# Kernel tuning notes

Measured on AMD Instinct MI355X. Metric: run time of the kernel, lower is better.

## Reference

```python
import jax, jax.numpy as jnp
import numpy as np

B, C, H, W = 4, 256, 64, 64
CH = C // 2  # inner channels


def setup_inputs() -> dict:
    key = jax.random.key(0)
    ks = jax.random.split(key, 9)
    s_in = 1.0 / np.sqrt(C)
    s_w = 1.0 / np.sqrt(CH)
    return {
        "x": jax.random.normal(ks[0], (B, C, H, W), dtype=jnp.float32),
        "theta_w": jax.random.normal(ks[1], (CH, C), dtype=jnp.float32) * s_in,
        "theta_b": jax.random.normal(ks[2], (CH,), dtype=jnp.float32) * s_in,
        "phi_w": jax.random.normal(ks[3], (CH, C), dtype=jnp.float32) * s_in,
        "phi_b": jax.random.normal(ks[4], (CH,), dtype=jnp.float32) * s_in,
        "g_w": jax.random.normal(ks[5], (CH, C), dtype=jnp.float32) * s_in,
        "g_b": jax.random.normal(ks[6], (CH,), dtype=jnp.float32) * s_in,
        "W_w": jax.random.normal(ks[7], (C, CH), dtype=jnp.float32) * s_w,
        "W_b": jax.random.normal(ks[8], (C,), dtype=jnp.float32) * s_w,
    }


def _proj(x_flat, w, b):
    # 1x1 conv == channel matmul; x_flat: [B, C, N] -> [B, O, N]
    return jnp.einsum("oc,bcn->bon", w, x_flat) + b[None, :, None]


def reference(x, theta_w, theta_b, phi_w, phi_b, g_w, g_b, W_w, W_b):
    b, c, h, w = x.shape
    n = h * w
    xf = x.reshape(b, c, n)
    theta = _proj(xf, theta_w, theta_b)  # [B, CH, N]
    phi = _proj(xf, phi_w, phi_b)        # [B, CH, N]
    g = _proj(xf, g_w, g_b)              # [B, CH, N]
    # scores[b,i,j] = theta[:, :, i] . phi[:, :, j]; softmax over j
    attn = jax.nn.softmax(jnp.einsum("bci,bcj->bij", theta, phi), axis=-1)
    # torch: bmm(g_x, attn) -> out[b,c,i] = sum_j g[b,c,j] * attn[b,j,i]
    out = jnp.einsum("bcj,bji->bci", g, attn)  # [B, CH, N]
    out = jnp.einsum("oc,bcn->bon", W_w, out) + W_b[None, :, None]
    return out.reshape(b, c, h, w) + x
```

## Files before the change

kernel.cpp:

```cpp
#include <hip/hip_runtime.h>
#include <hip/hip_bf16.h>
#include <math.h>

#define BB    4
#define CC    256
#define CHN   128
#define NN    4096

typedef short short8 __attribute__((ext_vector_type(8)));
typedef float f32x4  __attribute__((ext_vector_type(4)));
typedef float f32x16 __attribute__((ext_vector_type(16)));
typedef unsigned short u16;
typedef u16  us4 __attribute__((ext_vector_type(4)));

#define MFMA16(a, b, c) __builtin_amdgcn_mfma_f32_16x16x32_bf16((a), (b), (c), 0, 0, 0)
#define MFMA32(a, b, c) __builtin_amdgcn_mfma_f32_32x32x16_bf16((a), (b), (c), 0, 0, 0)
#define LOG2E 1.4426950408889634f

#if __has_builtin(__builtin_amdgcn_exp2f)
#define EXP2F(x) __builtin_amdgcn_exp2f(x)
#else
#define EXP2F(x) exp2f(x)
#endif
#if __has_builtin(__builtin_amdgcn_logf)
#define LOG2F(x) __builtin_amdgcn_logf(x)
#else
#define LOG2F(x) log2f(x)
#endif

static __device__ __forceinline__ u16 f2bf(float f) {
    union { float f; unsigned u; } v; v.f = f;
    unsigned r = v.u + 0x7FFFu + ((v.u >> 16) & 1u);
    return (u16)(r >> 16);
}
static __device__ __forceinline__ unsigned pkbf(float a, float b) {
    __hip_bfloat162 h = __float22bfloat162_rn(make_float2(a, b));
    return *reinterpret_cast<unsigned*>(&h);
}
static __device__ __forceinline__ int sw128(int row, int u) {
    return row * 128 + ((u ^ (row & 7)) << 3);
}
static __device__ __forceinline__ int sw64(int row, int u) {
    return row * 64 + ((u ^ (row & 7)) << 3);
}
static __device__ __forceinline__ void gload16(const u16* g, u16* l) {
    __builtin_amdgcn_global_load_lds(
        (const __attribute__((address_space(1))) void*)g,
        (__attribute__((address_space(3))) void*)l, 16, 0, 0);
}

typedef union { unsigned u[4]; short8 v; } bfrag;

#if __has_builtin(__builtin_amdgcn_permlane32_swap)
#define REPACK(sv, f) do { \
    unsigned e0 = pkbf(EXP2F(sv[0]),  EXP2F(sv[1])); \
    unsigned e1 = pkbf(EXP2F(sv[2]),  EXP2F(sv[3])); \
    unsigned e2 = pkbf(EXP2F(sv[4]),  EXP2F(sv[5])); \
    unsigned e3 = pkbf(EXP2F(sv[6]),  EXP2F(sv[7])); \
    unsigned e4 = pkbf(EXP2F(sv[8]),  EXP2F(sv[9])); \
    unsigned e5 = pkbf(EXP2F(sv[10]), EXP2F(sv[11])); \
    unsigned e6 = pkbf(EXP2F(sv[12]), EXP2F(sv[13])); \
    unsigned e7 = pkbf(EXP2F(sv[14]), EXP2F(sv[15])); \
    auto r02 = __builtin_amdgcn_permlane32_swap(e0, e2, false, false); \
    auto r13 = __builtin_amdgcn_permlane32_swap(e1, e3, false, false); \
    auto r46 = __builtin_amdgcn_permlane32_swap(e4, e6, false, false); \
    auto r57 = __builtin_amdgcn_permlane32_swap(e5, e7, false, false); \
    f[0].u[0] = r02[0]; f[0].u[1] = r13[0]; \
    f[0].u[2] = r02[1]; f[0].u[3] = r13[1]; \
    f[1].u[0] = r46[0]; f[1].u[1] = r57[0]; \
    f[1].u[2] = r46[1]; f[1].u[3] = r57[1]; \
} while (0)
#else
#define REPACK(sv, f) do { \
    unsigned e0 = pkbf(EXP2F(sv[0]),  EXP2F(sv[1])); \
    unsigned e1 = pkbf(EXP2F(sv[2]),  EXP2F(sv[3])); \
    unsigned e2 = pkbf(EXP2F(sv[4]),  EXP2F(sv[5])); \
    unsigned e3 = pkbf(EXP2F(sv[6]),  EXP2F(sv[7])); \
    unsigned e4 = pkbf(EXP2F(sv[8]),  EXP2F(sv[9])); \
    unsigned e5 = pkbf(EXP2F(sv[10]), EXP2F(sv[11])); \
    unsigned e6 = pkbf(EXP2F(sv[12]), EXP2F(sv[13])); \
    unsigned e7 = pkbf(EXP2F(sv[14]), EXP2F(sv[15])); \
    unsigned q0 = __shfl_xor(e0, 32), q1 = __shfl_xor(e1, 32); \
    unsigned q2 = __shfl_xor(e2, 32), q3 = __shfl_xor(e3, 32); \
    unsigned q4 = __shfl_xor(e4, 32), q5 = __shfl_xor(e5, 32); \
    unsigned q6 = __shfl_xor(e6, 32), q7 = __shfl_xor(e7, 32); \
    f[0].u[0] = lh ? q2 : e0;  f[0].u[1] = lh ? q3 : e1; \
    f[0].u[2] = lh ? e2 : q0;  f[0].u[3] = lh ? e3 : q1; \
    f[1].u[0] = lh ? q6 : e4;  f[1].u[1] = lh ? q7 : e5; \
    f[1].u[2] = lh ? e6 : q4;  f[1].u[3] = lh ? e7 : q5; \
} while (0)
#endif

__global__ __launch_bounds__(256) void k_cvtw(
    const float* __restrict__ tw, const float* __restrict__ pw,
    const float* __restrict__ gw, const float* __restrict__ Ww,
    u16* __restrict__ wall)
{
    int idx = (blockIdx.x * 256 + threadIdx.x) * 4;
    const float* s = (idx < 32768) ? tw
                   : (idx < 65536) ? pw
                   : (idx < 98304) ? gw : Ww;
    float sc = (idx < 32768) ? LOG2E : 1.0f;
    float4 v = *(const float4*)(s + (idx & 32767));
    us4 r = { f2bf(v.x * sc), f2bf(v.y * sc), f2bf(v.z * sc), f2bf(v.w * sc) };
    *(us4*)(wall + idx) = r;
}

__global__ __launch_bounds__(512) void k_proj(
    const float* __restrict__ x, const u16* __restrict__ wall,
    const float* __restrict__ tb, const float* __restrict__ pb,
    const float* __restrict__ gbias,
    u16* __restrict__ tht, u16* __restrict__ pht, u16* __restrict__ gg)
{
    __shared__ u16 xs[64 * 264];
    __shared__ u16 gbuf[128 * 68];
    const int tid = threadIdx.x;
    const int n0  = blockIdx.x * 64;
    const int b   = blockIdx.y;
    const int ln  = tid & 15, q = (tid >> 4) & 3, wid = tid >> 6;
    const int ow  = wid & 1, nw = wid >> 1;

    for (int p = 0; p < 8; ++p) {
        int id = p * 512 + tid;
        int c = id >> 4, n4 = (id & 15) * 4;
        float4 xv = *(const float4*)(x + ((size_t)b * CC + c) * NN + n0 + n4);
        xs[(n4 + 0) * 264 + c] = f2bf(xv.x);
        xs[(n4 + 1) * 264 + c] = f2bf(xv.y);
        xs[(n4 + 2) * 264 + c] = f2bf(xv.z);
        xs[(n4 + 3) * 264 + c] = f2bf(xv.w);
    }
    __syncthreads();

    short8 bfr[8];
    #pragma unroll
    for (int ks = 0; ks < 8; ++ks)
        bfr[ks] = *(const short8*)(&xs[(nw * 16 + ln) * 264 + ks * 32 + q * 8]);

    for (int pr = 0; pr < 3; ++pr) {
        const u16* wsrc = wall + pr * 32768;
        f32x4 acc[4];
        #pragma unroll
        for (int oo = 0; oo < 4; ++oo) acc[oo] = (f32x4){0.f, 0.f, 0.f, 0.f};
        for (int ks = 0; ks < 8; ++ks) {
            short8 a[4];
            #pragma unroll
            for (int oo = 0; oo < 4; ++oo)
                a[oo] = *(const short8*)(wsrc + (size_t)(ow*64 + oo*16 + ln) * 256 + ks*32 + q*8);
            #pragma unroll
            for (int oo = 0; oo < 4; ++oo)
                acc[oo] = MFMA16(a[oo], bfr[ks], acc[oo]);
        }
        const float* bias = (pr == 0) ? tb : (pr == 1 ? pb : gbias);
        const float bsc = (pr == 0) ? LOG2E : 1.0f;
        if (pr < 2) {
            u16* dst = (pr == 0) ? tht : pht;
            const int n = n0 + nw * 16 + ln;
            #pragma unroll
            for (int oo = 0; oo < 4; ++oo) {
                int o = ow * 64 + oo * 16 + q * 4;
                float4 bv = *(const float4*)(bias + o);
                f32x4 v = acc[oo];
                uint2 r = { pkbf(v.x + bv.x * bsc, v.y + bv.y * bsc),
                            pkbf(v.z + bv.z * bsc, v.w + bv.w * bsc) };
                *(uint2*)(dst + ((size_t)b * NN + n) * CHN + o) = r;
            }
        } else {
            const int nl = nw * 16 + ln;
            #pragma unroll
            for (int oo = 0; oo < 4; ++oo) {
                int o = ow * 64 + oo * 16 + q * 4;
                float4 bv = *(const float4*)(bias + o);
                f32x4 v = acc[oo];
                gbuf[(o + 0) * 68 + nl] = f2bf(v.x + bv.x);
                gbuf[(o + 1) * 68 + nl] = f2bf(v.y + bv.y);
                gbuf[(o + 2) * 68 + nl] = f2bf(v.z + bv.z);
                gbuf[(o + 3) * 68 + nl] = f2bf(v.w + bv.w);
            }
            __syncthreads();
            for (int p = 0; p < 4; ++p) {
                int id = p * 512 + tid;
                int c = id >> 4, n4 = (id & 15) * 4;
                us4 r = *(const us4*)(&gbuf[c * 68 + n4]);
                *(us4*)(gg + ((size_t)b * CHN + c) * NN + n0 + n4) = r;
            }
        }
    }
}

__global__ __launch_bounds__(512, 2) void k_rowsum(
    const u16* __restrict__ tht, const u16* __restrict__ pht,
    float* __restrict__ Z)
{
    __shared__ u16 ph_s[2][128 * 128];
    const int tid = threadIdx.x;
    const int j0  = blockIdx.x * 256;
    const int i00 = blockIdx.y * 1024;
    const int b   = blockIdx.z;
    const int l   = tid & 63, w = tid >> 6;
    const int lm  = l & 31, lh = l >> 5;
    const u16* thb = tht + (size_t)b * NN * CHN;
    const u16* phb = pht + (size_t)b * NN * CHN;

    short8 ar[8];
    #pragma unroll
    for (int ks = 0; ks < 8; ++ks)
        ar[ks] = *(const short8*)(thb + (size_t)(j0 + w*32 + lm) * CHN + ks*16 + lh*8);

    for (int p = 0; p < 4; ++p) {
        int id = p * 512 + tid;
        int row = id >> 4, u = id & 15;
        short8 v = *(const short8*)(phb + (size_t)(i00 + row) * CHN + u * 8);
        *(short8*)(&ph_s[0][sw128(row, u)]) = v;
    }

    float zp[16];
    #pragma unroll
    for (int r = 0; r < 16; ++r) zp[r] = 0.f;

    for (int is = 0; is < 8; ++is) {
        __syncthreads();
        if (is < 7) {
            for (int p = 0; p < 4; ++p) {
                int id = p * 512 + tid;
                int row = id >> 4, u = id & 15;
                short8 v = *(const short8*)(phb + (size_t)(i00 + (is+1)*128 + row) * CHN + u * 8);
                *(short8*)(&ph_s[(is + 1) & 1][sw128(row, u)]) = v;
            }
        }
        const u16* cur = ph_s[is & 1];

        #pragma unroll
        for (int ii = 0; ii < 4; ++ii) {
            f32x16 s;
            #pragma unroll
            for (int r = 0; r < 16; ++r) s[r] = 0.f;
            #pragma unroll
            for (int ks = 0; ks < 8; ++ks) {
                short8 bfrag = *(const short8*)(&cur[sw128(ii*32 + lm, ks*2 + lh)]);
                s = MFMA32(ar[ks], bfrag, s);
            }
            #pragma unroll
            for (int r = 0; r < 16; ++r) zp[r] += EXP2F(s[r]);
        }
    }

    float zr[16];
    #pragma unroll
    for (int r = 0; r < 16; ++r) {
        float v = zp[r];
        v += __shfl_xor(v, 1);
        v += __shfl_xor(v, 2);
        v += __shfl_xor(v, 4);
        v += __shfl_xor(v, 8);
        v += __shfl_xor(v, 16);
        zr[r] = v;
    }
    if (lm == 0) {
        #pragma unroll
        for (int r = 0; r < 16; ++r) {
            int j = j0 + w*32 + (r & 3) + 8*(r >> 2) + 4*lh;
            atomicAdd(&Z[(size_t)b * NN + j], zr[r]);
        }
    }
}

__global__ __launch_bounds__(256) void k_log(
    const float* __restrict__ Z, float* __restrict__ L)
{
    int idx = (blockIdx.x * 256 + threadIdx.x) * 4;
    float4 z = *(const float4*)(Z + idx);
    float4 r = { -LOG2F(z.x), -LOG2F(z.y), -LOG2F(z.z), -LOG2F(z.w) };
    *(float4*)(L + idx) = r;
}

__global__ __launch_bounds__(256) void k_attn(
    const u16* __restrict__ tht, const u16* __restrict__ pht,
    const u16* __restrict__ gg, const float* __restrict__ Lbuf,
    u16* __restrict__ innerT)
{
    __shared__ u16 th_s[2][64 * 128];
    __shared__ u16 g_s [2][128 * 64];
    const int tid = threadIdx.x;
    const int i0  = blockIdx.x * 256;
    const int jq  = blockIdx.y;
    const int b   = blockIdx.z;
    const int w   = tid >> 6;
    const int lm  = tid & 31, lh = (tid >> 5) & 1;

    const u16*  thb = tht + (size_t)b * NN * CHN;
    const u16*  ggb = gg  + (size_t)b * CHN * NN;
    const float* Lb = Lbuf + (size_t)b * NN;

    int offT[4], offG[4];
    #pragma unroll
    for (int p = 0; p < 4; ++p) {
        int id = p * 256 + tid;
        int rT = id >> 4, uT = (id & 15) ^ (rT & 7);
        offT[p] = rT * CHN + uT * 8;
        int rG = id >> 3, uG = (id & 7) ^ (rG & 7);
        offG[p] = rG * NN + uG * 8;
    }

    short8 phr[2][8];
    #pragma unroll
    for (int ih = 0; ih < 2; ++ih)
        #pragma unroll
        for (int ks = 0; ks < 8; ++ks)
            phr[ih][ks] = *(const short8*)(pht +
                ((size_t)b * NN + i0 + w*64 + ih*32 + lm) * CHN + ks*16 + lh*8);

    #pragma unroll
    for (int p = 0; p < 4; ++p) {
        gload16(thb + (size_t)(jq * 512) * CHN + offT[p], &th_s[0][0] + p*2048 + tid*8);
        gload16(ggb + jq * 512 + offG[p],                 &g_s [0][0] + p*2048 + tid*8);
    }
    __syncthreads();

    f32x16 pacc[4][2];
    #pragma unroll
    for (int ct = 0; ct < 4; ++ct)
        #pragma unroll
        for (int ih = 0; ih < 2; ++ih)
            #pragma unroll
            for (int r = 0; r < 16; ++r) pacc[ct][ih][r] = 0.f;

    for (int s = 0; s < 8; ++s) {
        const int j0s = jq * 512 + s * 64;
        const u16* thc = th_s[s & 1];
        const u16* gc  = g_s [s & 1];

        if (s < 7) {
            const int nb = (s + 1) & 1;
            #pragma unroll
            for (int p = 0; p < 4; ++p) {
                gload16(thb + (size_t)(j0s + 64) * CHN + offT[p], &th_s[nb][0] + p*2048 + tid*8);
                gload16(ggb + (j0s + 64) + offG[p],               &g_s [nb][0] + p*2048 + tid*8);
            }
        }

        #pragma unroll
        for (int jj = 0; jj < 2; ++jj) {
            f32x16 sv0;
            #pragma unroll
            for (int rq = 0; rq < 4; ++rq) {
                float4 Lv = *(const float4*)(Lb + j0s + jj*32 + rq*8 + lh*4);
                sv0[rq*4 + 0] = Lv.x; sv0[rq*4 + 1] = Lv.y;
                sv0[rq*4 + 2] = Lv.z; sv0[rq*4 + 3] = Lv.w;
            }
            f32x16 sv1 = sv0;
            #pragma unroll
            for (int ks = 0; ks < 8; ++ks) {
                short8 a = *(const short8*)(&thc[sw128(jj*32 + lm, ks*2 + lh)]);
                sv0 = MFMA32(a, phr[0][ks], sv0);
                sv1 = MFMA32(a, phr[1][ks], sv1);
            }
            bfrag fA[2], fB[2];
            REPACK(sv0, fA);
            REPACK(sv1, fB);
            #pragma unroll
            for (int h = 0; h < 2; ++h) {
                #pragma unroll
                for (int ct = 0; ct < 4; ++ct) {
                    short8 ag = *(const short8*)(&gc[sw64(ct*32 + lm, jj*4 + h*2 + lh)]);
                    pacc[ct][0] = MFMA32(ag, fA[h].v, pacc[ct][0]);
                    pacc[ct][1] = MFMA32(ag, fB[h].v, pacc[ct][1]);
                }
            }
        }
        __syncthreads();
    }

    u16* dst = innerT + ((size_t)jq * BB + b) * (size_t)NN * CHN;
    #pragma unroll
    for (int ct = 0; ct < 4; ++ct) {
        #pragma unroll
        for (int ih = 0; ih < 2; ++ih) {
            const int i = i0 + w*64 + ih*32 + lm;
            #pragma unroll
            for (int rq = 0; rq < 4; ++rq) {
                const int c0 = ct*32 + rq*8 + lh*4;
                uint2 r = { pkbf(pacc[ct][ih][rq*4+0], pacc[ct][ih][rq*4+1]),
                            pkbf(pacc[ct][ih][rq*4+2], pacc[ct][ih][rq*4+3]) };
                *(uint2*)(dst + (size_t)i * CHN + c0) = r;
            }
        }
    }
}

__global__ __launch_bounds__(512, 2) void k_final(
    const u16* __restrict__ innerT, const float* __restrict__ x,
    const u16* __restrict__ Wwbf, const float* __restrict__ Wb,
    float* __restrict__ out)
{
    __shared__ u16 w_s[256 * 128];
    __shared__ u16 a_s[64 * 128];
    const int tid = threadIdx.x;
    const int n0  = blockIdx.x * 64;
    const int b   = blockIdx.y;
    const int l   = tid & 63, w = tid >> 6;
    const int lm  = l & 31, lh = l >> 5;

    for (int p = 0; p < 8; ++p) {
        int id = p * 512 + tid;
        int row = id >> 4, u = id & 15;
        *(short8*)(&w_s[sw128(row, u)]) = *(const short8*)(Wwbf + (size_t)row * CHN + u * 8);
    }
    __syncthreads();

    short8 aw[8];
    #pragma unroll
    for (int ks = 0; ks < 8; ++ks)
        aw[ks] = *(const short8*)(&w_s[sw128(w*32 + lm, ks*2 + lh)]);

    f32x16 acc[2];
    #pragma unroll
    for (int nt = 0; nt < 2; ++nt)
        #pragma unroll
        for (int r = 0; r < 16; ++r) acc[nt][r] = 0.f;

    for (int jq = 0; jq < 8; ++jq) {
        __syncthreads();
        for (int p = 0; p < 2; ++p) {
            int id = p * 512 + tid;
            int row = id >> 4, u = id & 15;
            *(short8*)(&a_s[sw128(row, u)]) =
                *(const short8*)(innerT + (((size_t)jq * BB + b) * NN + n0 + row) * CHN + u * 8);
        }
        __syncthreads();
        #pragma unroll
        for (int ks = 0; ks < 8; ++ks) {
            short8 bn[2];
            #pragma unroll
            for (int nt = 0; nt < 2; ++nt)
                bn[nt] = *(const short8*)(&a_s[sw128(nt*32 + lm, ks*2 + lh)]);
            acc[0] = MFMA32(aw[ks], bn[0], acc[0]);
            acc[1] = MFMA32(aw[ks], bn[1], acc[1]);
        }
    }

    #pragma unroll
    for (int nt = 0; nt < 2; ++nt) {
        const int n = n0 + nt*32 + lm;
        #pragma unroll
        for (int r = 0; r < 16; ++r) {
            const int o = w*32 + (r & 3) + 8*(r >> 2) + 4*lh;
            const size_t idx = ((size_t)b * CC + o) * NN + n;
            out[idx] = acc[nt][r] + Wb[o] + x[idx];
        }
    }
}

extern "C" void kernel_launch(void* const* d_in, const int* in_sizes, int n_in,
                              void* d_out, int out_size, void* d_ws, size_t ws_size,
                              hipStream_t stream)
{
    const float* x  = (const float*)d_in[0];
    const float* tw = (const float*)d_in[1];
    const float* tb = (const float*)d_in[2];
    const float* pw = (const float*)d_in[3];
    const float* pb = (const float*)d_in[4];
    const float* gw = (const float*)d_in[5];
    const float* gb = (const float*)d_in[6];
    const float* Ww = (const float*)d_in[7];
    const float* Wb = (const float*)d_in[8];
    float* out = (float*)d_out;

    char* p = (char*)d_ws;
    const size_t proj_u16 = (size_t)BB * NN * CHN;
    u16*   tht    = (u16*)p;   p += proj_u16 * 2;
    u16*   pht    = (u16*)p;   p += proj_u16 * 2;
    u16*   gg     = (u16*)p;   p += proj_u16 * 2;
    u16*   wall   = (u16*)p;   p += (size_t)131072 * 2;
    float* Z      = (float*)p; p += (size_t)BB * NN * 4;
    float* Lbuf   = (float*)p; p += (size_t)BB * NN * 4;
    u16*   innerT = (u16*)p;

    hipMemsetAsync(Z, 0, (size_t)BB * NN * sizeof(float), stream);
    k_cvtw  <<<128, 256, 0, stream>>>(tw, pw, gw, Ww, wall);
    k_proj  <<<dim3(64, BB), 512, 0, stream>>>(x, wall, tb, pb, gb, tht, pht, gg);
    k_rowsum<<<dim3(16, 4, BB), 512, 0, stream>>>(tht, pht, Z);
    k_log   <<<16, 256, 0, stream>>>(Z, Lbuf);
    k_attn  <<<dim3(16, 8, BB), 256, 0, stream>>>(tht, pht, gg, Lbuf, innerT);
    k_final <<<dim3(64, BB), 512, 0, stream>>>(innerT, x, wall + 98304, Wb, out);
}
```

Baseline: 210.8 us.

## Add 512-thread attention variant with larger j-slabs, chosen by register count

Adds k_attn_a, an attention kernel with 512 threads where each wave owns 32 query rows and the block handles 1024-key slabs. The grid halves along j, so k_final reduces only 4 partial slabs instead of 8. At first launch the host reads k_attn_b's register count and keeps the original kernel only if it uses at least 240 registers. The aim is to avoid register spilling or low occupancy in the old kernel and to cut partial-sum traffic, at the cost of 128 KB of LDS per block and more per-block serial work.

```diff
diff --git a/kernel.cpp b/kernel.cpp
--- a/kernel.cpp
+++ b/kernel.cpp
@@ -273,7 +273,108 @@
     *(float4*)(L + idx) = r;
 }
 
-__global__ __launch_bounds__(256) void k_attn(
+__global__ __launch_bounds__(512, 2) void k_attn_a(
+    const u16* __restrict__ tht, const u16* __restrict__ pht,
+    const u16* __restrict__ gg, const float* __restrict__ Lbuf,
+    u16* __restrict__ innerT)
+{
+    __shared__ u16 th_s[2][128 * 128];
+    __shared__ u16 g_s [2][128 * 128];
+    const int tid = threadIdx.x;
+    const int i0  = blockIdx.x * 256;
+    const int jq  = blockIdx.y;
+    const int b   = blockIdx.z;
+    const int w   = tid >> 6;
+    const int lm  = tid & 31, lh = (tid >> 5) & 1;
+
+    const u16*  thb = tht + (size_t)b * NN * CHN;
+    const u16*  ggb = gg  + (size_t)b * CHN * NN;
+    const float* Lb = Lbuf + (size_t)b * NN;
+
+    int offT[4], offG[4];
+    #pragma unroll
+    for (int p = 0; p < 4; ++p) {
+        int row = p * 32 + (tid >> 4);
+        int u   = (tid & 15) ^ (row & 7);
+        offT[p] = row * CHN + u * 8;
+        offG[p] = row * NN  + u * 8;
+    }
+
+    short8 phr[8];
+    #pragma unroll
+    for (int ks = 0; ks < 8; ++ks)
+        phr[ks] = *(const short8*)(pht + ((size_t)b * NN + i0 + w*32 + lm) * CHN + ks*16 + lh*8);
+
+    #pragma unroll
+    for (int p = 0; p < 4; ++p) {
+        gload16(thb + (size_t)(jq * 1024) * CHN + offT[p], &th_s[0][0] + p*4096 + (w << 9));
+        gload16(ggb + jq * 1024 + offG[p],                 &g_s [0][0] + p*4096 + (w << 9));
+    }
+    __syncthreads();
+
+    f32x16 pacc[4];
+    #pragma unroll
+    for (int ct = 0; ct < 4; ++ct)
+        #pragma unroll
+        for (int r = 0; r < 16; ++r) pacc[ct][r] = 0.f;
+
+    for (int s = 0; s < 8; ++s) {
+        const int j0s = jq * 1024 + s * 128;
+        const u16* thc = th_s[s & 1];
+        const u16* gc  = g_s [s & 1];
+
+        if (s < 7) {
+            const int nb = (s + 1) & 1;
+            #pragma unroll
+            for (int p = 0; p < 4; ++p) {
+                gload16(thb + (size_t)(j0s + 128) * CHN + offT[p], &th_s[nb][0] + p*4096 + (w << 9));
+                gload16(ggb + (j0s + 128) + offG[p],               &g_s [nb][0] + p*4096 + (w << 9));
+            }
+        }
+
+        #pragma unroll
+        for (int jj = 0; jj < 4; ++jj) {
+            f32x16 sv;
+            #pragma unroll
+            for (int rq = 0; rq < 4; ++rq) {
+                float4 Lv = *(const float4*)(Lb + j0s + jj*32 + rq*8 + lh*4);
+                sv[rq*4 + 0] = Lv.x; sv[rq*4 + 1] = Lv.y;
+                sv[rq*4 + 2] = Lv.z; sv[rq*4 + 3] = Lv.w;
+            }
+            #pragma unroll
+            for (int ks = 0; ks < 8; ++ks) {
+                short8 a = *(const short8*)(&thc[sw128(jj*32 + lm, ks*2 + lh)]);
+                sv = MFMA32(a, phr[ks], sv);
+            }
+            bfrag f[2];
+            REPACK(sv, f);
+            #pragma unroll
+            for (int h = 0; h < 2; ++h) {
+                #pragma unroll
+                for (int ct = 0; ct < 4; ++ct) {
+                    short8 ag = *(const short8*)(&gc[sw128(ct*32 + lm, jj*4 + h*2 + lh)]);
+                    pacc[ct] = MFMA32(ag, f[h].v, pacc[ct]);
+                }
+            }
+        }
+        __syncthreads();
+    }
+
+    u16* dst = innerT + ((size_t)jq * BB + b) * (size_t)NN * CHN;
+    const int i = i0 + w*32 + lm;
+    #pragma unroll
+    for (int ct = 0; ct < 4; ++ct) {
+        #pragma unroll
+        for (int rq = 0; rq < 4; ++rq) {
+            const int c0 = ct*32 + rq*8 + lh*4;
+            uint2 r = { pkbf(pacc[ct][rq*4+0], pacc[ct][rq*4+1]),
+                        pkbf(pacc[ct][rq*4+2], pacc[ct][rq*4+3]) };
+            *(uint2*)(dst + (size_t)i * CHN + c0) = r;
+        }
+    }
+}
+
+__global__ __launch_bounds__(256, 1) void k_attn_b(
     const u16* __restrict__ tht, const u16* __restrict__ pht,
     const u16* __restrict__ gg, const float* __restrict__ Lbuf,
     u16* __restrict__ innerT)
@@ -361,11 +462,12 @@
             for (int h = 0; h < 2; ++h) {
                 #pragma unroll
                 for (int ct = 0; ct < 4; ++ct) {
-                    short8 ag = *(const short8*)(&gc[sw64(ct*32 + lm, jj*4 + h*2 + lh)]);
+                    short8 ag = *(const short8*)(&g_s[s & 1][sw64(ct*32 + lm, jj*4 + h*2 + lh)]);
                     pacc[ct][0] = MFMA32(ag, fA[h].v, pacc[ct][0]);
                     pacc[ct][1] = MFMA32(ag, fB[h].v, pacc[ct][1]);
                 }
             }
+            (void)gc;
         }
         __syncthreads();
     }
@@ -390,7 +492,7 @@
 __global__ __launch_bounds__(512, 2) void k_final(
     const u16* __restrict__ innerT, const float* __restrict__ x,
     const u16* __restrict__ Wwbf, const float* __restrict__ Wb,
-    float* __restrict__ out)
+    float* __restrict__ out, int nslab)
 {
     __shared__ u16 w_s[256 * 128];
     __shared__ u16 a_s[64 * 128];
@@ -418,7 +520,7 @@
         #pragma unroll
         for (int r = 0; r < 16; ++r) acc[nt][r] = 0.f;
 
-    for (int jq = 0; jq < 8; ++jq) {
+    for (int jq = 0; jq < nslab; ++jq) {
         __syncthreads();
         for (int p = 0; p < 2; ++p) {
             int id = p * 512 + tid;
@@ -465,6 +567,13 @@
     const float* Wb = (const float*)d_in[8];
     float* out = (float*)d_out;
 
+    static int use_b = -1;
+    if (use_b < 0) {
+        hipFuncAttributes attr;
+        use_b = (hipFuncGetAttributes(&attr, (const void*)k_attn_b) == hipSuccess
+                 && attr.numRegs >= 240) ? 1 : 0;
+    }
+
     char* p = (char*)d_ws;
     const size_t proj_u16 = (size_t)BB * NN * CHN;
     u16*   tht    = (u16*)p;   p += proj_u16 * 2;
@@ -480,6 +589,11 @@
     k_proj  <<<dim3(64, BB), 512, 0, stream>>>(x, wall, tb, pb, gb, tht, pht, gg);
     k_rowsum<<<dim3(16, 4, BB), 512, 0, stream>>>(tht, pht, Z);
     k_log   <<<16, 256, 0, stream>>>(Z, Lbuf);
-    k_attn  <<<dim3(16, 8, BB), 256, 0, stream>>>(tht, pht, gg, Lbuf, innerT);
-    k_final <<<dim3(64, BB), 512, 0, stream>>>(innerT, x, wall + 98304, Wb, out);
-}
+    if (use_b) {
+        k_attn_b<<<dim3(16, 8, BB), 256, 0, stream>>>(tht, pht, gg, Lbuf, innerT);
+        k_final <<<dim3(64, BB), 512, 0, stream>>>(innerT, x, wall + 98304, Wb, out, 8);
+    } else {
+        k_attn_a<<<dim3(16, 4, BB), 512, 0, stream>>>(tht, pht, gg, Lbuf, innerT);
+        k_final <<<dim3(64, BB), 512, 0, stream>>>(innerT, x, wall + 98304, Wb, out, 4);
+    }
+}
```

Result: no change. 210.2 us (-0.3%).
